# Performance work log

Hardware: AMD Instinct MI355X
Metric: run time of the kernel (lower is better)

The kernel has to match this reference:

```python
import jax, jax.numpy as jnp
import numpy as np

# ---- dims ----
N = 16380      # atoms
R = 819        # residues
APR = 20       # atoms per residue
K = 16         # k_neighbors
H = 64         # hidden_mult (channels)
HEADS = 8
DH = H // HEADS
L = 6          # hidden_layers
BINS = 100
MIN_D, MAX_D = 0.0, 10.0
E_DIM = 64     # embed_dim
FFN = 2 * H    # mlp_ratio = 2


def setup_inputs() -> dict:
    key = jax.random.key(0)
    ks = jax.random.split(key, 22)
    g = lambda k, shape, fan: jax.random.normal(k, shape, jnp.float32) / np.sqrt(fan)
    return {
        'coords': jax.random.uniform(ks[0], (N, 3), jnp.float32) * 70.0,
        'atom_ids': jax.random.randint(ks[1], (N,), 0, 64),
        'res_ids': jax.random.randint(ks[2], (N,), 0, 8),
        'elem_ids': jax.random.randint(ks[3], (N,), 0, 16),
        'residue_index': jnp.repeat(jnp.arange(R), APR),
        'emb_atom': jax.random.normal(ks[4], (64, 32), jnp.float32),
        'emb_res': jax.random.normal(ks[5], (8, 16), jnp.float32),
        'emb_elem': jax.random.normal(ks[6], (16, 16), jnp.float32),
        'Win': g(ks[7], (E_DIM, H), E_DIM),
        'Wq': g(ks[8], (L, H, H), H),
        'Wk': g(ks[9], (L, H, H), H),
        'Wv': g(ks[10], (L, H, H), H),
        'Wvec': g(ks[11], (L, H, H), H),
        'wdir': jax.random.normal(ks[12], (L, H), jnp.float32) * 0.1,
        'dist_bias': jax.random.normal(ks[13], (L, BINS, HEADS), jnp.float32) * 0.1,
        'Wo': g(ks[14], (L, H, H), H),
        'W1': g(ks[15], (L, H, FFN), H),
        'W2': g(ks[16], (L, FFN, H), FFN),
        'Wg': g(ks[17], (L, H, H), H),
        'Wout': g(ks[18], (H, 2), H),
        'bout': jnp.zeros((2,), jnp.float32),
    }


def _ln(x):
    m = jnp.mean(x, axis=-1, keepdims=True)
    v = jnp.mean((x - m) ** 2, axis=-1, keepdims=True)
    return (x - m) * jax.lax.rsqrt(v + 1e-5)


def reference(coords, atom_ids, res_ids, elem_ids, residue_index,
              emb_atom, emb_res, emb_elem, Win, Wq, Wk, Wv, Wvec, wdir,
              dist_bias, Wo, W1, W2, Wg, Wout, bout):
    n = coords.shape[0]
    # --- polymer embedding: concat atom/residue/element embeddings ---
    feat = jnp.concatenate(
        [emb_atom[atom_ids], emb_res[res_ids], emb_elem[elem_ids]], axis=-1)  # (N, E_DIM)
    # --- kNN graph via dense pairwise distances (avoid (N,N,3) intermediate) ---
    sq = jnp.sum(coords * coords, axis=-1)
    d2 = sq[:, None] + sq[None, :] - 2.0 * (coords @ coords.T)     # (N, N)
    idx = jnp.arange(n)
    d2 = d2.at[idx, idx].set(jnp.inf)
    _, nbr = jax.lax.top_k(-d2, K)                                  # (N, K) src per dst
    # --- edge geometry: relative vector, distance, bin ---
    dvec = coords[:, None, :] - coords[nbr]                         # (N, K, 3) dst - src
    d = jnp.sqrt(jnp.sum(dvec * dvec, axis=-1) + 1e-12)
    dirn = dvec / d[..., None]
    bins = jnp.clip(((d - MIN_D) / (MAX_D - MIN_D) * BINS).astype(jnp.int32), 0, BINS - 1)
    # --- lift to hidden repr: scalars from embedding, vectors start at zero ---
    s = feat @ Win                                                  # (N, H) l=0 features
    v = jnp.zeros((n, H, 3), s.dtype)                               # (N, H, 3) l=1 features
    for l in range(L):
        h = _ln(s)
        q = (h @ Wq[l]).reshape(n, HEADS, DH)
        kf = (h @ Wk[l]).reshape(n, HEADS, DH)
        vf = (h @ Wv[l]).reshape(n, HEADS, DH)
        kn, vn = kf[nbr], vf[nbr]                                   # (N, K, HEADS, DH)
        logits = jnp.einsum('nhd,nkhd->nkh', q, kn) / np.sqrt(DH) + dist_bias[l][bins]
        attn = jax.nn.softmax(logits, axis=1)                       # softmax over K nbrs
        msg = jnp.einsum('nkh,nkhd->nhd', attn, vn).reshape(n, H)
        # equivariant vector messages: mixed source vectors + edge direction term
        vvals = jnp.einsum('nhc,hg->ngc', v, Wvec[l])               # (N, H, 3)
        vmsg = vvals[nbr] + wdir[l][None, None, :, None] * dirn[:, :, None, :]
        attn_c = jnp.repeat(attn, DH, axis=-1)                      # (N, K, H)
        vagg = jnp.einsum('nkh,nkhc->nhc', attn_c, vmsg)
        s = s + msg @ Wo[l]
        v = v + vagg
        h2 = _ln(s)
        s = s + jax.nn.gelu(h2 @ W1[l]) @ W2[l]                     # scalar FFN
        v = v * jax.nn.sigmoid(h2 @ Wg[l])[..., None]               # gated vector update
    # --- out repr is l=0 only; residue mean-pool then linear head ---
    res_feat = jax.ops.segment_sum(s, residue_index, num_segments=R) / APR
    return res_feat @ Wout + bout                                   # (R, 2)
```

## Files before the change

### kernel.cpp

```cpp
#include <hip/hip_runtime.h>
#include <cfloat>

#define NN    16380
#define RR    819
#define APR   20
#define KNB   16
#define HID   64
#define LAYERS 6
#define BINS  100
#define N64   (NN*HID)

#define ATB   32
#define NBLK  512
#define LDA   68
#define LDU   132
#define CSIZE 4.375f

#define OFF_QA    0
#define OFF_KA    (1*N64)
#define OFF_FA    (2*N64)
#define OFF_QB    (3*N64)
#define OFF_KB    (4*N64)
#define OFF_FB    (5*N64)
#define OFF_VA    (6*N64)
#define OFF_VB    (9*N64)
#define OFF_S     (12*N64)
#define OFF_DIRNS (13*N64)
#define OFF_C4    (OFF_DIRNS + NN*48)
#define OFF_C4S   (OFF_C4 + NN*4)
#define OFF_RES   (OFF_C4S + NN*4)
#define OFF_NBRS  (OFF_RES + RR*64)
#define OFF_BINSS (OFF_NBRS + NN*16)
#define OFF_O2N   (OFF_BINSS + NN*16)
#define OFF_N2O   (OFF_O2N + NN)
#define OFF_CELL  (OFF_N2O + NN)
#define OFF_HIST  (OFF_CELL + NN)
#define OFF_CNT   (OFF_HIST + 4096)
#define OFF_BASE  (OFF_CNT + 4096)

typedef unsigned long long u64;
#define U64MAX 0xFFFFFFFFFFFFFFFFull

__device__ __forceinline__ float gelu_f(float x) {
    float x3 = x*x*x;
    float t = tanhf(0.7978845608028654f*(x + 0.044715f*x3));
    return 0.5f*x*(1.0f+t);
}
__device__ __forceinline__ float sigmoid_f(float x) {
    return 1.0f/(1.0f + expf(-x));
}
__device__ __forceinline__ int spread3(int x) {
    return (x&1) | ((x&2)<<2) | ((x&4)<<4) | ((x&8)<<6);
}
__device__ __forceinline__ unsigned sortable_u32(float f) {
    unsigned u = __float_as_uint(f);
    return u ^ ((u & 0x80000000u) ? 0xFFFFFFFFu : 0x80000000u);
}

__global__ void pad_cell_kernel(const float* __restrict__ coords, float4* __restrict__ c4,
                                int* __restrict__ cellid, int* __restrict__ hist,
                                float* __restrict__ resb, int n) {
    int i = blockIdx.x*256 + threadIdx.x;
    for (int j = i; j < RR*HID; j += 16384) resb[j] = 0.f;
    if (i >= n) return;
    float x = coords[3*i], y = coords[3*i+1], z = coords[3*i+2];
    float sq = __fadd_rn(__fadd_rn(__fmul_rn(x,x), __fmul_rn(y,y)), __fmul_rn(z,z));
    c4[i] = make_float4(x, y, z, sq);
    int cx = min(15, max(0, (int)(x * (16.0f/70.0f))));
    int cy = min(15, max(0, (int)(y * (16.0f/70.0f))));
    int cz = min(15, max(0, (int)(z * (16.0f/70.0f))));
    int m = spread3(cx) | (spread3(cy)<<1) | (spread3(cz)<<2);
    cellid[i] = m;
    atomicAdd(&hist[m], 1);
}
__global__ void scan_kernel(const int* __restrict__ hist, int* __restrict__ base) {
    __shared__ int part[256];
    int t = threadIdx.x;
    int loc[16]; int s = 0;
    #pragma unroll
    for (int e = 0; e < 16; ++e) { loc[e] = s; s += hist[t*16+e]; }
    part[t] = s;
    __syncthreads();
    if (t == 0) { int acc = 0; for (int i = 0; i < 256; ++i) { int v = part[i]; part[i] = acc; acc += v; } }
    __syncthreads();
    int off = part[t];
    #pragma unroll
    for (int e = 0; e < 16; ++e) base[t*16+e] = off + loc[e];
}
__global__ void scatter_kernel(const int* __restrict__ cellid, const int* __restrict__ base,
                               int* __restrict__ cnt, int* __restrict__ o2n,
                               int* __restrict__ n2o, const float4* __restrict__ c4,
                               float4* __restrict__ c4s, int n) {
    int i = blockIdx.x*256 + threadIdx.x;
    if (i >= n) return;
    int m = cellid[i];
    int pos = base[m] + atomicAdd(&cnt[m], 1);
    o2n[i] = pos; n2o[pos] = i;
    c4s[pos] = c4[i];
}

#define SCRATCH 1024
__global__ __launch_bounds__(256) void knn_grid_kernel(
    const float4* __restrict__ c4s, const int* __restrict__ base, const int* __restrict__ hist,
    const int* __restrict__ n2o, const int* __restrict__ o2n,
    int* __restrict__ nbr, int* __restrict__ binsO, float* __restrict__ dirn, int n)
{
    __shared__ int sIdx[4][SCRATCH];
    int tid = threadIdx.x;
    int wv = tid >> 6, lane = tid & 63;
    int i = blockIdx.x*4 + wv;
    bool valid = i < n;
    int ii = valid ? i : 0;
    float4 cd = c4s[ii];
    float sqd = cd.w;
    int cx = min(15, max(0, (int)(cd.x * (16.0f/70.0f))));
    int cy = min(15, max(0, (int)(cd.y * (16.0f/70.0f))));
    int cz = min(15, max(0, (int)(cd.z * (16.0f/70.0f))));
    u64 dlist = U64MAX;
    u64 vmax  = U64MAX;
    int* sidx = sIdx[wv];

    auto compute_pk = [&](int idx) -> u64 {
        if (idx == i) return U64MAX;
        float4 cc = c4s[idx];
        float dt = __fmul_rn(cd.x, cc.x);
        dt = __fmaf_rn(cd.y, cc.y, dt);
        dt = __fmaf_rn(cd.z, cc.z, dt);
        float key = __fsub_rn(__fadd_rn(sqd, cc.w), __fmul_rn(2.0f, dt));
        int org = n2o[idx];
        return ((u64)sortable_u32(key) << 32) | (unsigned)org;
    };

    auto process_batch = [&](int M) {
        if (M <= 0) return;
        u64 lmin = U64MAX;
        for (int p = lane; p < M; p += 64) {
            u64 pk = compute_pk(sidx[p]);
            lmin = (pk < lmin) ? pk : lmin;
        }
        u64 T = lmin;
        #pragma unroll
        for (int off = 1; off < 64; off <<= 1) {
            u64 o = __shfl_xor(T, off);
            T = (o > T) ? o : T;
        }
        for (int c0 = 0; c0 < M; c0 += 64) {
            int p = c0 + lane;
            u64 mypk = (p < M) ? compute_pk(sidx[p]) : U64MAX;
            u64 bound = (vmax < T) ? vmax : T;
            unsigned long long mask = __ballot(mypk <= bound);
            while (mask) {
                int lb = (int)__builtin_ctzll(mask);
                mask &= mask - 1;
                u64 dc = __shfl(mypk, lb);
                if (dc < vmax) {
                    u64 dp = __shfl_up(dlist, 1);
                    bool below = dc < dlist;
                    bool take  = below && (lane == 0 || dc >= dp);
                    if (lane < 16) dlist = below ? (take ? dc : dp) : dlist;
                    vmax = __shfl(dlist, 15);
                }
            }
        }
    };

    for (int R = 2; R <= 16; ++R) {
        int side = 2*R+1;
        int ncell = side*side*side;
        int M = 0;
        for (int t0 = 0; t0 < ncell; t0 += 64) {
            int t = t0 + lane;
            int cnt = 0, b = 0;
            if (t < ncell) {
                int dxc = t % side - R;
                int dyc = (t/side) % side - R;
                int dzc = t/(side*side) - R;
                int ch = max(abs(dxc), max(abs(dyc), abs(dzc)));
                bool use = (R == 2) || (ch == R);
                int x = cx+dxc, y = cy+dyc, z = cz+dzc;
                if (use && x>=0 && x<16 && y>=0 && y<16 && z>=0 && z<16) {
                    int m = spread3(x) | (spread3(y)<<1) | (spread3(z)<<2);
                    cnt = hist[m]; b = base[m];
                }
            }
            int incl = cnt;
            #pragma unroll
            for (int o = 1; o < 64; o <<= 1) { int v = __shfl_up(incl, o); if (lane >= o) incl += v; }
            int excl = incl - cnt;
            int tot = __shfl(incl, 63);
            if (M + tot > SCRATCH) { process_batch(M); M = 0; }
            for (int e = 0; e < cnt; ++e) {
                int pos = M + excl + e;
                if (pos < SCRATCH) sidx[pos] = b + e;
            }
            M = min(M + tot, SCRATCH);
        }
        process_batch(M);
        float rim = (float)R * CSIZE;
        unsigned thS = sortable_u32(rim*rim - 0.05f);
        if ((unsigned)(vmax >> 32) < thS) break;
    }
    if (valid && lane < 16) {
        int org = (int)(dlist & 0xFFFFFFFFull);
        int src = o2n[org];
        float4 cs = c4s[src];
        float dx = __fsub_rn(cd.x, cs.x);
        float dy = __fsub_rn(cd.y, cs.y);
        float dz = __fsub_rn(cd.z, cs.z);
        float ss = __fadd_rn(__fadd_rn(__fmul_rn(dx,dx), __fmul_rn(dy,dy)),
                             __fmul_rn(dz,dz));
        float dd = __fsqrt_rn(__fadd_rn(ss, 1e-12f));
        nbr[i*KNB + lane] = src;
        float bf = __fmul_rn(__fdiv_rn(dd, 10.0f), 100.0f);
        int b = (int)bf;
        b = min(max(b, 0), BINS-1);
        binsO[i*KNB + lane] = b;
        dirn[i*48 + lane*3 + 0] = __fdiv_rn(dx, dd);
        dirn[i*48 + lane*3 + 1] = __fdiv_rn(dy, dd);
        dirn[i*48 + lane*3 + 2] = __fdiv_rn(dz, dd);
    }
}

__global__ __launch_bounds__(256) void prologue_kernel(
    const int* __restrict__ aid, const int* __restrict__ rid, const int* __restrict__ eid,
    const int* __restrict__ n2o,
    const float* __restrict__ ea, const float* __restrict__ er, const float* __restrict__ ee,
    const float* __restrict__ Win, const float* __restrict__ Wq, const float* __restrict__ Wk,
    const float* __restrict__ Wv,
    float* __restrict__ sg, float* __restrict__ qout, float* __restrict__ kout,
    float* __restrict__ vfout)
{
    __shared__ __align__(16) float sS[ATB*LDA];
    __shared__ __align__(16) float sH[ATB*LDA];
    __shared__ __align__(16) float sW[4096];
    const int tid = threadIdx.x;
    const int a0 = blockIdx.x*ATB;
    const int gi = tid>>4, gj = tid&15;
    const int lrow = tid>>3, lsub = tid&7;

    auto stageW = [&](const float* W) {
        const float4* src = (const float4*)W; float4* dst = (float4*)sW;
        #pragma unroll
        for (int r = 0; r < 4; ++r) dst[tid + 256*r] = src[tid + 256*r];
    };
    auto do_gemm = [&](const float* sA, float4& c0, float4& c1) {
        const float* a0p = sA + gi*LDA;
        const float* a1p = sA + (gi+16)*LDA;
        const float* wr  = sW + gj*4;
        #pragma unroll 8
        for (int k = 0; k < 64; ++k) {
            float av0 = a0p[k], av1 = a1p[k];
            float4 w = *(const float4*)(wr + k*64);
            c0.x = fmaf(av0,w.x,c0.x); c0.y = fmaf(av0,w.y,c0.y);
            c0.z = fmaf(av0,w.z,c0.z); c0.w = fmaf(av0,w.w,c0.w);
            c1.x = fmaf(av1,w.x,c1.x); c1.y = fmaf(av1,w.y,c1.y);
            c1.z = fmaf(av1,w.z,c1.z); c1.w = fmaf(av1,w.w,c1.w);
        }
    };
    auto do_ln = [&](const float* src, float* dst) {
        const float* sp = src + lrow*LDA + lsub*8;
        float v[8]; float s1 = 0.f;
        #pragma unroll
        for (int e = 0; e < 8; ++e) { v[e] = sp[e]; s1 += v[e]; }
        s1 += __shfl_xor(s1,1); s1 += __shfl_xor(s1,2); s1 += __shfl_xor(s1,4);
        float mean = s1*(1.0f/64.0f);
        float s2 = 0.f;
        #pragma unroll
        for (int e = 0; e < 8; ++e) { float t = v[e]-mean; s2 += t*t; }
        s2 += __shfl_xor(s2,1); s2 += __shfl_xor(s2,2); s2 += __shfl_xor(s2,4);
        float sc = 1.0f/sqrtf(s2*(1.0f/64.0f)+1e-5f);
        float* dp = dst + lrow*LDA + lsub*8;
        #pragma unroll
        for (int e = 0; e < 8; ++e) dp[e] = (v[e]-mean)*sc;
    };
    auto store_g = [&](float* base, float4 c0, float4 c1) {
        int g0 = a0+gi, g1 = a0+gi+16;
        if (g0 < NN) *(float4*)(base + (size_t)g0*64 + gj*4) = c0;
        if (g1 < NN) *(float4*)(base + (size_t)g1*64 + gj*4) = c1;
    };

    {
        int ga = a0 + lrow;
        int io = (ga < NN) ? n2o[ga] : 0;
        #pragma unroll
        for (int e = 0; e < 8; ++e) {
            int c = lsub*8 + e;
            float x = 0.f;
            if (ga < NN) {
                if (c < 32)      x = ea[aid[io]*32 + c];
                else if (c < 48) x = er[rid[io]*16 + (c-32)];
                else             x = ee[eid[io]*16 + (c-48)];
            }
            sH[lrow*LDA + c] = x;
        }
    }
    __syncthreads();
    stageW(Win); __syncthreads();
    {
        float4 c0 = make_float4(0,0,0,0), c1 = c0;
        do_gemm(sH, c0, c1);
        *(float4*)(sS + gi*LDA + gj*4)      = c0;
        *(float4*)(sS + (gi+16)*LDA + gj*4) = c1;
        store_g(sg, c0, c1);
    }
    __syncthreads();
    do_ln(sS, sH);
    __syncthreads();
    stageW(Wk); __syncthreads();
    { float4 c0 = make_float4(0,0,0,0), c1 = c0; do_gemm(sH, c0, c1); store_g(kout, c0, c1); }
    __syncthreads();
    stageW(Wv); __syncthreads();
    { float4 c0 = make_float4(0,0,0,0), c1 = c0; do_gemm(sH, c0, c1); store_g(vfout, c0, c1); }
    __syncthreads();
    stageW(Wq); __syncthreads();
    { float4 c0 = make_float4(0,0,0,0), c1 = c0; do_gemm(sH, c0, c1); store_g(qout, c0, c1); }
}

__global__ __launch_bounds__(256) void layer_kernel(
    const float* __restrict__ qin, const float* __restrict__ kin, const float* __restrict__ vfin,
    float* __restrict__ qout, float* __restrict__ kout, float* __restrict__ vfout,
    const float* __restrict__ vin, float* __restrict__ vout,
    float* __restrict__ sg, const float* __restrict__ dirn,
    const int* __restrict__ nbr, const int* __restrict__ bins,
    float* __restrict__ resb, const int* __restrict__ ridx, const int* __restrict__ n2o,
    const float* __restrict__ Wvec, const float* __restrict__ wdir,
    const float* __restrict__ dist_bias,
    const float* __restrict__ Wo, const float* __restrict__ W1, const float* __restrict__ W2,
    const float* __restrict__ Wg, const float* __restrict__ Wq, const float* __restrict__ Wk,
    const float* __restrict__ Wv, int l)
{
    __shared__ __align__(16) float sS[ATB*LDA];
    __shared__ __align__(16) float sH[ATB*LDA];
    __shared__ __align__(16) float sM[ATB*LDU];
    __shared__ __align__(16) float sVA[3][ATB*LDA];
    __shared__ __align__(16) float sW[4096];
    __shared__ float sDS[ATB*24];

    const int tid = threadIdx.x;
    const int bswz = (blockIdx.x & 7) * (NBLK/8) + (blockIdx.x >> 3);
    const int a0 = bswz*ATB;
    const int gi = tid>>4, gj = tid&15;
    const int lrow = tid>>3, lsub = tid&7;
    const int wv = tid>>6, lane = tid&63;

    const float* Wo_l = Wo + l*4096;
    const float* Wg_l = Wg + l*4096;
    const float* Wc_l = Wvec + l*4096;
    const float* W1_l = W1 + l*8192;
    const float* W2_l = W2 + l*8192;
    const float* db_l = dist_bias + l*BINS*8;
    const float* wd_l = wdir + l*64;

    auto stageW = [&](const float* W) {
        const float4* src = (const float4*)W; float4* dst = (float4*)sW;
        #pragma unroll
        for (int r = 0; r < 4; ++r) dst[tid + 256*r] = src[tid + 256*r];
    };
    auto stageW1h = [&](const float* W1l, int h) {
        const float4* src = (const float4*)W1l; float4* dst = (float4*)sW;
        #pragma unroll
        for (int r = 0; r < 4; ++r) {
            int q = tid + 256*r;
            int row = q >> 4, c4i = q & 15;
            dst[q] = src[row*32 + h*16 + c4i];
        }
    };
    auto do_gemm = [&](const float* sA, int lda, int ko, float4& c0, float4& c1) {
        const float* a0p = sA + gi*lda + ko;
        const float* a1p = sA + (gi+16)*lda + ko;
        const float* wr  = sW + gj*4;
        #pragma unroll 8
        for (int k = 0; k < 64; ++k) {
            float av0 = a0p[k], av1 = a1p[k];
            float4 w = *(const float4*)(wr + k*64);
            c0.x = fmaf(av0,w.x,c0.x); c0.y = fmaf(av0,w.y,c0.y);
            c0.z = fmaf(av0,w.z,c0.z); c0.w = fmaf(av0,w.w,c0.w);
            c1.x = fmaf(av1,w.x,c1.x); c1.y = fmaf(av1,w.y,c1.y);
            c1.z = fmaf(av1,w.z,c1.z); c1.w = fmaf(av1,w.w,c1.w);
        }
    };
    auto do_ln = [&](const float* src, float* dst) {
        const float* sp = src + lrow*LDA + lsub*8;
        float v[8]; float s1 = 0.f;
        #pragma unroll
        for (int e = 0; e < 8; ++e) { v[e] = sp[e]; s1 += v[e]; }
        s1 += __shfl_xor(s1,1); s1 += __shfl_xor(s1,2); s1 += __shfl_xor(s1,4);
        float mean = s1*(1.0f/64.0f);
        float s2 = 0.f;
        #pragma unroll
        for (int e = 0; e < 8; ++e) { float t = v[e]-mean; s2 += t*t; }
        s2 += __shfl_xor(s2,1); s2 += __shfl_xor(s2,2); s2 += __shfl_xor(s2,4);
        float sc = 1.0f/sqrtf(s2*(1.0f/64.0f)+1e-5f);
        float* dp = dst + lrow*LDA + lsub*8;
        #pragma unroll
        for (int e = 0; e < 8; ++e) dp[e] = (v[e]-mean)*sc;
    };
    auto store_g = [&](float* base, float4 c0, float4 c1) {
        int g0 = a0+gi, g1 = a0+gi+16;
        if (g0 < NN) *(float4*)(base + (size_t)g0*64 + gj*4) = c0;
        if (g1 < NN) *(float4*)(base + (size_t)g1*64 + gj*4) = c1;
    };

    {
        int ga = a0 + lrow;
        float4 z = make_float4(0,0,0,0);
        float4 x0 = z, x1 = z;
        if (ga < NN) {
            const float4* sp = (const float4*)(sg + (size_t)ga*64);
            x0 = sp[lsub*2]; x1 = sp[lsub*2+1];
        }
        float4* dp = (float4*)(sS + lrow*LDA);
        dp[lsub*2] = x0; dp[lsub*2+1] = x1;
    }

    for (int aa = 0; aa < 8; ++aa) {
        int la = wv*8 + aa;
        int ga = a0 + la;
        if (ga >= NN) break;
        float qh = qin[(size_t)ga*64 + lane];
        float lg[KNB]; int nb[KNB];
        #pragma unroll
        for (int k = 0; k < KNB; ++k) {
            int j = nbr[ga*KNB + k];
            nb[k] = j;
            float t = qh * kin[(size_t)j*64 + lane];
            t += __shfl_xor(t,1); t += __shfl_xor(t,2); t += __shfl_xor(t,4);
            lg[k] = t*0.35355339059327373f + db_l[bins[ga*KNB+k]*8 + (lane>>3)];
        }
        float m = lg[0];
        #pragma unroll
        for (int k = 1; k < KNB; ++k) m = fmaxf(m, lg[k]);
        float ssum = 0.f;
        #pragma unroll
        for (int k = 0; k < KNB; ++k) { lg[k] = expf(lg[k]-m); ssum += lg[k]; }
        float inv = 1.0f/ssum;
        float mh=0.f, b0=0.f, b1=0.f, b2=0.f, s0=0.f, s1=0.f, s2=0.f;
        if (l > 0) {
            #pragma unroll
            for (int k = 0; k < KNB; ++k) {
                float w = lg[k]*inv; int j = nb[k];
                mh += w * vfin[(size_t)j*64 + lane];
                b0 += w * vin[(size_t)j*64 + lane];
                b1 += w * vin[(size_t)N64 + (size_t)j*64 + lane];
                b2 += w * vin[2*(size_t)N64 + (size_t)j*64 + lane];
                s0 += w * dirn[ga*48 + k*3 + 0];
                s1 += w * dirn[ga*48 + k*3 + 1];
                s2 += w * dirn[ga*48 + k*3 + 2];
            }
            sVA[0][la*LDA + lane] = b0;
            sVA[1][la*LDA + lane] = b1;
            sVA[2][la*LDA + lane] = b2;
        } else {
            #pragma unroll
            for (int k = 0; k < KNB; ++k) {
                float w = lg[k]*inv; int j = nb[k];
                mh += w * vfin[(size_t)j*64 + lane];
                s0 += w * dirn[ga*48 + k*3 + 0];
                s1 += w * dirn[ga*48 + k*3 + 1];
                s2 += w * dirn[ga*48 + k*3 + 2];
            }
        }
        sM[la*LDU + lane] = mh;
        if ((lane & 7) == 0) {
            int hh = lane >> 3;
            sDS[la*24 + 0*8 + hh] = s0;
            sDS[la*24 + 1*8 + hh] = s1;
            sDS[la*24 + 2*8 + hh] = s2;
        }
    }
    __syncthreads();

    stageW(Wo_l); __syncthreads();
    {
        float4 c0 = *(float4*)(sS + gi*LDA + gj*4);
        float4 c1 = *(float4*)(sS + (gi+16)*LDA + gj*4);
        do_gemm(sM, LDU, 0, c0, c1);
        __syncthreads();
        *(float4*)(sS + gi*LDA + gj*4)      = c0;
        *(float4*)(sS + (gi+16)*LDA + gj*4) = c1;
    }
    __syncthreads();

    do_ln(sS, sH);
    __syncthreads();

    stageW(Wg_l); __syncthreads();
    {
        float4 g0 = make_float4(0,0,0,0), g1 = g0;
        do_gemm(sH, LDA, 0, g0, g1);
        g0.x=sigmoid_f(g0.x); g0.y=sigmoid_f(g0.y); g0.z=sigmoid_f(g0.z); g0.w=sigmoid_f(g0.w);
        g1.x=sigmoid_f(g1.x); g1.y=sigmoid_f(g1.y); g1.z=sigmoid_f(g1.z); g1.w=sigmoid_f(g1.w);
        __syncthreads();
        stageW(Wc_l); __syncthreads();
        float4 wd4 = *(const float4*)&wd_l[gj*4];
        int g0i = a0+gi, g1i = a0+gi+16;
        #pragma unroll
        for (int p = 0; p < 3; ++p) {
            float4 t0 = make_float4(0,0,0,0), t1 = t0;
            if (l > 0) do_gemm(sVA[p], LDA, 0, t0, t1);
            float sp0 = sDS[gi*24 + p*8 + (gj>>1)];
            float sp1 = sDS[(gi+16)*24 + p*8 + (gj>>1)];
            if (g0i < NN) {
                float4 vi = make_float4(0,0,0,0);
                if (l > 0) vi = *(const float4*)(vin + (size_t)p*N64 + (size_t)g0i*64 + gj*4);
                float4 o;
                o.x = (vi.x + t0.x + wd4.x*sp0)*g0.x;
                o.y = (vi.y + t0.y + wd4.y*sp0)*g0.y;
                o.z = (vi.z + t0.z + wd4.z*sp0)*g0.z;
                o.w = (vi.w + t0.w + wd4.w*sp0)*g0.w;
                *(float4*)(vout + (size_t)p*N64 + (size_t)g0i*64 + gj*4) = o;
            }
            if (g1i < NN) {
                float4 vi = make_float4(0,0,0,0);
                if (l > 0) vi = *(const float4*)(vin + (size_t)p*N64 + (size_t)g1i*64 + gj*4);
                float4 o;
                o.x = (vi.x + t1.x + wd4.x*sp1)*g1.x;
                o.y = (vi.y + t1.y + wd4.y*sp1)*g1.y;
                o.z = (vi.z + t1.z + wd4.z*sp1)*g1.z;
                o.w = (vi.w + t1.w + wd4.w*sp1)*g1.w;
                *(float4*)(vout + (size_t)p*N64 + (size_t)g1i*64 + gj*4) = o;
            }
        }
    }
    __syncthreads();

    stageW1h(W1_l, 0); __syncthreads();
    {
        float4 c0 = make_float4(0,0,0,0), c1 = c0;
        do_gemm(sH, LDA, 0, c0, c1);
        c0.x=gelu_f(c0.x); c0.y=gelu_f(c0.y); c0.z=gelu_f(c0.z); c0.w=gelu_f(c0.w);
        c1.x=gelu_f(c1.x); c1.y=gelu_f(c1.y); c1.z=gelu_f(c1.z); c1.w=gelu_f(c1.w);
        __syncthreads();
        *(float4*)(sM + gi*LDU + gj*4)      = c0;
        *(float4*)(sM + (gi+16)*LDU + gj*4) = c1;
    }
    __syncthreads();
    stageW1h(W1_l, 1); __syncthreads();
    {
        float4 c0 = make_float4(0,0,0,0), c1 = c0;
        do_gemm(sH, LDA, 0, c0, c1);
        c0.x=gelu_f(c0.x); c0.y=gelu_f(c0.y); c0.z=gelu_f(c0.z); c0.w=gelu_f(c0.w);
        c1.x=gelu_f(c1.x); c1.y=gelu_f(c1.y); c1.z=gelu_f(c1.z); c1.w=gelu_f(c1.w);
        __syncthreads();
        *(float4*)(sM + gi*LDU + 64 + gj*4)      = c0;
        *(float4*)(sM + (gi+16)*LDU + 64 + gj*4) = c1;
    }
    __syncthreads();
    stageW(W2_l); __syncthreads();
    {
        float4 c0 = *(float4*)(sS + gi*LDA + gj*4);
        float4 c1 = *(float4*)(sS + (gi+16)*LDA + gj*4);
        do_gemm(sM, LDU, 0, c0, c1);
        __syncthreads();
        stageW(W2_l + 4096); __syncthreads();
        do_gemm(sM, LDU, 64, c0, c1);
        __syncthreads();
        *(float4*)(sS + gi*LDA + gj*4)      = c0;
        *(float4*)(sS + (gi+16)*LDA + gj*4) = c1;
    }
    __syncthreads();

    if (l < LAYERS-1) {
        do_ln(sS, sH);
        __syncthreads();
        stageW(Wk + (l+1)*4096); __syncthreads();
        { float4 c0 = make_float4(0,0,0,0), c1 = c0; do_gemm(sH, LDA, 0, c0, c1); store_g(kout, c0, c1); }
        __syncthreads();
        stageW(Wv + (l+1)*4096); __syncthreads();
        { float4 c0 = make_float4(0,0,0,0), c1 = c0; do_gemm(sH, LDA, 0, c0, c1); store_g(vfout, c0, c1); }
        __syncthreads();
        stageW(Wq + (l+1)*4096); __syncthreads();
        { float4 c0 = make_float4(0,0,0,0), c1 = c0; do_gemm(sH, LDA, 0, c0, c1); store_g(qout, c0, c1); }
        {
            int ga = a0 + lrow;
            if (ga < NN) {
                float4* dp = (float4*)(sg + (size_t)ga*64);
                const float4* sp = (const float4*)(sS + lrow*LDA);
                dp[lsub*2] = sp[lsub*2]; dp[lsub*2+1] = sp[lsub*2+1];
            }
        }
    } else {
        int ga = a0 + lrow;
        if (ga < NN) {
            int r = ridx[n2o[ga]];
            #pragma unroll
            for (int e = 0; e < 8; ++e)
                atomicAdd(&resb[r*64 + lsub*8 + e], sS[lrow*LDA + lsub*8 + e]);
        }
    }
}

__global__ void head_kernel(const float* __restrict__ res, const float* __restrict__ Wout,
                            const float* __restrict__ bout, float* __restrict__ out, int r_total) {
    int wave = threadIdx.x >> 6, lane = threadIdx.x & 63;
    int r = blockIdx.x*4 + wave;
    if (r >= r_total) return;
    float p = res[r*HID + lane] * (1.0f/APR);
    float o0 = p * Wout[lane*2 + 0];
    float o1 = p * Wout[lane*2 + 1];
    #pragma unroll
    for (int off = 1; off < 64; off <<= 1) { o0 += __shfl_xor(o0, off); o1 += __shfl_xor(o1, off); }
    if (lane == 0) { out[r*2+0] = o0 + bout[0]; out[r*2+1] = o1 + bout[1]; }
}

extern "C" void kernel_launch(void* const* d_in, const int* in_sizes, int n_in,
                              void* d_out, int out_size, void* d_ws, size_t ws_size,
                              hipStream_t stream) {
    const float* coords    = (const float*)d_in[0];
    const int*   atom_ids  = (const int*)d_in[1];
    const int*   res_ids   = (const int*)d_in[2];
    const int*   elem_ids  = (const int*)d_in[3];
    const int*   ridx      = (const int*)d_in[4];
    const float* emb_atom  = (const float*)d_in[5];
    const float* emb_res   = (const float*)d_in[6];
    const float* emb_elem  = (const float*)d_in[7];
    const float* Win       = (const float*)d_in[8];
    const float* Wq        = (const float*)d_in[9];
    const float* Wk        = (const float*)d_in[10];
    const float* Wv        = (const float*)d_in[11];
    const float* Wvec      = (const float*)d_in[12];
    const float* wdir      = (const float*)d_in[13];
    const float* dist_bias = (const float*)d_in[14];
    const float* Wo        = (const float*)d_in[15];
    const float* W1        = (const float*)d_in[16];
    const float* W2        = (const float*)d_in[17];
    const float* Wg        = (const float*)d_in[18];
    const float* Wout      = (const float*)d_in[19];
    const float* bout      = (const float*)d_in[20];
    float* out = (float*)d_out;

    float* ws = (float*)d_ws;
    float* qA = ws + OFF_QA;  float* kA = ws + OFF_KA;  float* fA = ws + OFF_FA;
    float* qB = ws + OFF_QB;  float* kB = ws + OFF_KB;  float* fB = ws + OFF_FB;
    float* vA = ws + OFF_VA;  float* vB = ws + OFF_VB;
    float* sg = ws + OFF_S;
    float* dirn_s = ws + OFF_DIRNS;
    float4* c4  = (float4*)(ws + OFF_C4);
    float4* c4s = (float4*)(ws + OFF_C4S);
    float* resb = ws + OFF_RES;
    int* nbr_s  = (int*)(ws + OFF_NBRS);
    int* bins_s = (int*)(ws + OFF_BINSS);
    int* o2n    = (int*)(ws + OFF_O2N);
    int* n2o    = (int*)(ws + OFF_N2O);
    int* cellid = (int*)(ws + OFF_CELL);
    int* hist   = (int*)(ws + OFF_HIST);
    int* cnt    = (int*)(ws + OFF_CNT);
    int* baseb  = (int*)(ws + OFF_BASE);

    hipMemsetAsync(hist, 0, 2*4096*sizeof(int), stream);

    pad_cell_kernel<<<(NN+255)/256, 256, 0, stream>>>(coords, c4, cellid, hist, resb, NN);
    scan_kernel<<<1, 256, 0, stream>>>(hist, baseb);
    scatter_kernel<<<(NN+255)/256, 256, 0, stream>>>(cellid, baseb, cnt, o2n, n2o, c4, c4s, NN);
    knn_grid_kernel<<<(NN+3)/4, 256, 0, stream>>>(c4s, baseb, hist, n2o, o2n, nbr_s, bins_s, dirn_s, NN);

    prologue_kernel<<<NBLK, 256, 0, stream>>>(atom_ids, res_ids, elem_ids, n2o,
                                              emb_atom, emb_res, emb_elem,
                                              Win, Wq, Wk, Wv, sg, qA, kA, fA);
    for (int l = 0; l < LAYERS; ++l) {
        int p = l & 1;
        const float* qin = p ? qB : qA;  float* qout = p ? qA : qB;
        const float* kin = p ? kB : kA;  float* kout = p ? kA : kB;
        const float* fin = p ? fB : fA;  float* fout = p ? fA : fB;
        const float* vin = p ? vB : vA;  float* vout = p ? vA : vB;
        layer_kernel<<<NBLK, 256, 0, stream>>>(qin, kin, fin, qout, kout, fout,
                                               vin, vout, sg, dirn_s, nbr_s, bins_s,
                                               resb, ridx, n2o,
                                               Wvec, wdir, dist_bias,
                                               Wo, W1, W2, Wg, Wq, Wk, Wv, l);
    }
    head_kernel<<<(RR+3)/4, 256, 0, stream>>>(resb, Wout, bout, out, RR);
}
```

Before: 620.6 us.

## Fuse prologue, all layers and head into one persistent kernel with grid barriers

Merges the prologue, the six per-layer launches and the head kernel into a single persistent kernel of 512 blocks. Between stages it uses an atomic counter and generation software grid barrier in workspace, which is zeroed by the extended memset. This removes seven kernel launch gaps and tail drains. In exchange it depends on all 512 blocks being co-resident to avoid deadlock, and it spins on global atomics at every layer boundary.

```diff
diff --git a/kernel.cpp b/kernel.cpp
--- a/kernel.cpp
+++ b/kernel.cpp
@@ -37,6 +37,7 @@
 #define OFF_HIST  (OFF_CELL + NN)
 #define OFF_CNT   (OFF_HIST + 4096)
 #define OFF_BASE  (OFF_CNT + 4096)
+#define OFF_BAR   (OFF_BASE + 4096)
 
 typedef unsigned long long u64;
 #define U64MAX 0xFFFFFFFFFFFFFFFFull
@@ -221,31 +222,53 @@
     }
 }
 
-__global__ __launch_bounds__(256) void prologue_kernel(
+__global__ __launch_bounds__(256) void mega_kernel(
     const int* __restrict__ aid, const int* __restrict__ rid, const int* __restrict__ eid,
-    const int* __restrict__ n2o,
+    const int* __restrict__ n2o, const int* __restrict__ ridx,
     const float* __restrict__ ea, const float* __restrict__ er, const float* __restrict__ ee,
     const float* __restrict__ Win, const float* __restrict__ Wq, const float* __restrict__ Wk,
-    const float* __restrict__ Wv,
-    float* __restrict__ sg, float* __restrict__ qout, float* __restrict__ kout,
-    float* __restrict__ vfout)
+    const float* __restrict__ Wv, const float* __restrict__ Wvec, const float* __restrict__ wdir,
+    const float* __restrict__ dist_bias, const float* __restrict__ Wo,
+    const float* __restrict__ W1, const float* __restrict__ W2, const float* __restrict__ Wg,
+    const float* __restrict__ Wout, const float* __restrict__ bout,
+    float* __restrict__ qA, float* __restrict__ kA, float* __restrict__ fA,
+    float* __restrict__ qB, float* __restrict__ kB, float* __restrict__ fB,
+    float* __restrict__ vA, float* __restrict__ vB,
+    float* __restrict__ sg, const float* __restrict__ dirn,
+    const int* __restrict__ nbr, const int* __restrict__ bins,
+    float* __restrict__ resb, unsigned* __restrict__ bar, float* __restrict__ out)
 {
     __shared__ __align__(16) float sS[ATB*LDA];
     __shared__ __align__(16) float sH[ATB*LDA];
+    __shared__ __align__(16) float sM[ATB*LDU];
+    __shared__ __align__(16) float sVA[3][ATB*LDA];
     __shared__ __align__(16) float sW[4096];
+    __shared__ float sDS[ATB*24];
+
     const int tid = threadIdx.x;
-    const int a0 = blockIdx.x*ATB;
+    const int bswz = (blockIdx.x & 7) * (NBLK/8) + (blockIdx.x >> 3);
+    const int a0 = bswz*ATB;
     const int gi = tid>>4, gj = tid&15;
     const int lrow = tid>>3, lsub = tid&7;
+    const int wv = tid>>6, lane = tid&63;
 
     auto stageW = [&](const float* W) {
         const float4* src = (const float4*)W; float4* dst = (float4*)sW;
         #pragma unroll
         for (int r = 0; r < 4; ++r) dst[tid + 256*r] = src[tid + 256*r];
     };
-    auto do_gemm = [&](const float* sA, float4& c0, float4& c1) {
-        const float* a0p = sA + gi*LDA;
-        const float* a1p = sA + (gi+16)*LDA;
+    auto stageW1h = [&](const float* W1l, int h) {
+        const float4* src = (const float4*)W1l; float4* dst = (float4*)sW;
+        #pragma unroll
+        for (int r = 0; r < 4; ++r) {
+            int q = tid + 256*r;
+            int row = q >> 4, c4i = q & 15;
+            dst[q] = src[row*32 + h*16 + c4i];
+        }
+    };
+    auto do_gemm = [&](const float* sA, int lda, int ko, float4& c0, float4& c1) {
+        const float* a0p = sA + gi*lda + ko;
+        const float* a1p = sA + (gi+16)*lda + ko;
         const float* wr  = sW + gj*4;
         #pragma unroll 8
         for (int k = 0; k < 64; ++k) {
@@ -278,6 +301,23 @@
         if (g0 < NN) *(float4*)(base + (size_t)g0*64 + gj*4) = c0;
         if (g1 < NN) *(float4*)(base + (size_t)g1*64 + gj*4) = c1;
     };
+    auto grid_sync = [&]() {
+        __syncthreads();
+        __threadfence();
+        if (tid == 0) {
+            unsigned* cnt = bar; unsigned* gen = bar+1;
+            unsigned g = __hip_atomic_load(gen, __ATOMIC_RELAXED, __HIP_MEMORY_SCOPE_AGENT);
+            unsigned arr = __hip_atomic_fetch_add(cnt, 1u, __ATOMIC_ACQ_REL, __HIP_MEMORY_SCOPE_AGENT);
+            if (arr == (unsigned)(NBLK-1)) {
+                __hip_atomic_store(cnt, 0u, __ATOMIC_RELAXED, __HIP_MEMORY_SCOPE_AGENT);
+                __hip_atomic_fetch_add(gen, 1u, __ATOMIC_RELEASE, __HIP_MEMORY_SCOPE_AGENT);
+            } else {
+                while (__hip_atomic_load(gen, __ATOMIC_ACQUIRE, __HIP_MEMORY_SCOPE_AGENT) == g) {}
+            }
+        }
+        __syncthreads();
+        __threadfence();
+    };
 
     {
         int ga = a0 + lrow;
@@ -298,7 +338,7 @@
     stageW(Win); __syncthreads();
     {
         float4 c0 = make_float4(0,0,0,0), c1 = c0;
-        do_gemm(sH, c0, c1);
+        do_gemm(sH, LDA, 0, c0, c1);
         *(float4*)(sS + gi*LDA + gj*4)      = c0;
         *(float4*)(sS + (gi+16)*LDA + gj*4) = c1;
         store_g(sg, c0, c1);
@@ -307,300 +347,237 @@
     do_ln(sS, sH);
     __syncthreads();
     stageW(Wk); __syncthreads();
-    { float4 c0 = make_float4(0,0,0,0), c1 = c0; do_gemm(sH, c0, c1); store_g(kout, c0, c1); }
+    { float4 c0 = make_float4(0,0,0,0), c1 = c0; do_gemm(sH, LDA, 0, c0, c1); store_g(kA, c0, c1); }
     __syncthreads();
     stageW(Wv); __syncthreads();
-    { float4 c0 = make_float4(0,0,0,0), c1 = c0; do_gemm(sH, c0, c1); store_g(vfout, c0, c1); }
+    { float4 c0 = make_float4(0,0,0,0), c1 = c0; do_gemm(sH, LDA, 0, c0, c1); store_g(fA, c0, c1); }
     __syncthreads();
     stageW(Wq); __syncthreads();
-    { float4 c0 = make_float4(0,0,0,0), c1 = c0; do_gemm(sH, c0, c1); store_g(qout, c0, c1); }
-}
-
-__global__ __launch_bounds__(256) void layer_kernel(
-    const float* __restrict__ qin, const float* __restrict__ kin, const float* __restrict__ vfin,
-    float* __restrict__ qout, float* __restrict__ kout, float* __restrict__ vfout,
-    const float* __restrict__ vin, float* __restrict__ vout,
-    float* __restrict__ sg, const float* __restrict__ dirn,
-    const int* __restrict__ nbr, const int* __restrict__ bins,
-    float* __restrict__ resb, const int* __restrict__ ridx, const int* __restrict__ n2o,
-    const float* __restrict__ Wvec, const float* __restrict__ wdir,
-    const float* __restrict__ dist_bias,
-    const float* __restrict__ Wo, const float* __restrict__ W1, const float* __restrict__ W2,
-    const float* __restrict__ Wg, const float* __restrict__ Wq, const float* __restrict__ Wk,
-    const float* __restrict__ Wv, int l)
-{
-    __shared__ __align__(16) float sS[ATB*LDA];
-    __shared__ __align__(16) float sH[ATB*LDA];
-    __shared__ __align__(16) float sM[ATB*LDU];
-    __shared__ __align__(16) float sVA[3][ATB*LDA];
-    __shared__ __align__(16) float sW[4096];
-    __shared__ float sDS[ATB*24];
-
-    const int tid = threadIdx.x;
-    const int bswz = (blockIdx.x & 7) * (NBLK/8) + (blockIdx.x >> 3);
-    const int a0 = bswz*ATB;
-    const int gi = tid>>4, gj = tid&15;
-    const int lrow = tid>>3, lsub = tid&7;
-    const int wv = tid>>6, lane = tid&63;
-
-    const float* Wo_l = Wo + l*4096;
-    const float* Wg_l = Wg + l*4096;
-    const float* Wc_l = Wvec + l*4096;
-    const float* W1_l = W1 + l*8192;
-    const float* W2_l = W2 + l*8192;
-    const float* db_l = dist_bias + l*BINS*8;
-    const float* wd_l = wdir + l*64;
-
-    auto stageW = [&](const float* W) {
-        const float4* src = (const float4*)W; float4* dst = (float4*)sW;
-        #pragma unroll
-        for (int r = 0; r < 4; ++r) dst[tid + 256*r] = src[tid + 256*r];
-    };
-    auto stageW1h = [&](const float* W1l, int h) {
-        const float4* src = (const float4*)W1l; float4* dst = (float4*)sW;
-        #pragma unroll
-        for (int r = 0; r < 4; ++r) {
-            int q = tid + 256*r;
-            int row = q >> 4, c4i = q & 15;
-            dst[q] = src[row*32 + h*16 + c4i];
-        }
-    };
-    auto do_gemm = [&](const float* sA, int lda, int ko, float4& c0, float4& c1) {
-        const float* a0p = sA + gi*lda + ko;
-        const float* a1p = sA + (gi+16)*lda + ko;
-        const float* wr  = sW + gj*4;
-        #pragma unroll 8
-        for (int k = 0; k < 64; ++k) {
-            float av0 = a0p[k], av1 = a1p[k];
-            float4 w = *(const float4*)(wr + k*64);
-            c0.x = fmaf(av0,w.x,c0.x); c0.y = fmaf(av0,w.y,c0.y);
-            c0.z = fmaf(av0,w.z,c0.z); c0.w = fmaf(av0,w.w,c0.w);
-            c1.x = fmaf(av1,w.x,c1.x); c1.y = fmaf(av1,w.y,c1.y);
-            c1.z = fmaf(av1,w.z,c1.z); c1.w = fmaf(av1,w.w,c1.w);
-        }
-    };
-    auto do_ln = [&](const float* src, float* dst) {
-        const float* sp = src + lrow*LDA + lsub*8;
-        float v[8]; float s1 = 0.f;
-        #pragma unroll
-        for (int e = 0; e < 8; ++e) { v[e] = sp[e]; s1 += v[e]; }
-        s1 += __shfl_xor(s1,1); s1 += __shfl_xor(s1,2); s1 += __shfl_xor(s1,4);
-        float mean = s1*(1.0f/64.0f);
-        float s2 = 0.f;
-        #pragma unroll
-        for (int e = 0; e < 8; ++e) { float t = v[e]-mean; s2 += t*t; }
-        s2 += __shfl_xor(s2,1); s2 += __shfl_xor(s2,2); s2 += __shfl_xor(s2,4);
-        float sc = 1.0f/sqrtf(s2*(1.0f/64.0f)+1e-5f);
-        float* dp = dst + lrow*LDA + lsub*8;
-        #pragma unroll
-        for (int e = 0; e < 8; ++e) dp[e] = (v[e]-mean)*sc;
-    };
-    auto store_g = [&](float* base, float4 c0, float4 c1) {
-        int g0 = a0+gi, g1 = a0+gi+16;
-        if (g0 < NN) *(float4*)(base + (size_t)g0*64 + gj*4) = c0;
-        if (g1 < NN) *(float4*)(base + (size_t)g1*64 + gj*4) = c1;
-    };
-
-    {
-        int ga = a0 + lrow;
-        float4 z = make_float4(0,0,0,0);
-        float4 x0 = z, x1 = z;
-        if (ga < NN) {
-            const float4* sp = (const float4*)(sg + (size_t)ga*64);
-            x0 = sp[lsub*2]; x1 = sp[lsub*2+1];
-        }
-        float4* dp = (float4*)(sS + lrow*LDA);
-        dp[lsub*2] = x0; dp[lsub*2+1] = x1;
-    }
-
-    for (int aa = 0; aa < 8; ++aa) {
-        int la = wv*8 + aa;
-        int ga = a0 + la;
-        if (ga >= NN) break;
-        float qh = qin[(size_t)ga*64 + lane];
-        float lg[KNB]; int nb[KNB];
-        #pragma unroll
-        for (int k = 0; k < KNB; ++k) {
-            int j = nbr[ga*KNB + k];
-            nb[k] = j;
-            float t = qh * kin[(size_t)j*64 + lane];
-            t += __shfl_xor(t,1); t += __shfl_xor(t,2); t += __shfl_xor(t,4);
-            lg[k] = t*0.35355339059327373f + db_l[bins[ga*KNB+k]*8 + (lane>>3)];
-        }
-        float m = lg[0];
-        #pragma unroll
-        for (int k = 1; k < KNB; ++k) m = fmaxf(m, lg[k]);
-        float ssum = 0.f;
-        #pragma unroll
-        for (int k = 0; k < KNB; ++k) { lg[k] = expf(lg[k]-m); ssum += lg[k]; }
-        float inv = 1.0f/ssum;
-        float mh=0.f, b0=0.f, b1=0.f, b2=0.f, s0=0.f, s1=0.f, s2=0.f;
-        if (l > 0) {
+    { float4 c0 = make_float4(0,0,0,0), c1 = c0; do_gemm(sH, LDA, 0, c0, c1); store_g(qA, c0, c1); }
+
+    grid_sync();
+
+    for (int l = 0; l < LAYERS; ++l) {
+        int par = l & 1;
+        const float* qin  = par ? qB : qA;
+        const float* kin  = par ? kB : kA;
+        const float* vfin = par ? fB : fA;
+        float* qout = par ? qA : qB;
+        float* kout = par ? kA : kB;
+        float* vfout= par ? fA : fB;
+        const float* vin = par ? vB : vA;
+        float* vout      = par ? vA : vB;
+
+        const float* Wo_l = Wo + l*4096;
+        const float* Wg_l = Wg + l*4096;
+        const float* Wc_l = Wvec + l*4096;
+        const float* W1_l = W1 + l*8192;
+        const float* W2_l = W2 + l*8192;
+        const float* db_l = dist_bias + l*BINS*8;
+        const float* wd_l = wdir + l*64;
+
+        {
+            int ga = a0 + lrow;
+            float4 z = make_float4(0,0,0,0);
+            float4 x0 = z, x1 = z;
+            if (ga < NN) {
+                const float4* sp = (const float4*)(sg + (size_t)ga*64);
+                x0 = sp[lsub*2]; x1 = sp[lsub*2+1];
+            }
+            float4* dp = (float4*)(sS + lrow*LDA);
+            dp[lsub*2] = x0; dp[lsub*2+1] = x1;
+        }
+
+        for (int aa = 0; aa < 8; ++aa) {
+            int la = wv*8 + aa;
+            int ga = a0 + la;
+            if (ga >= NN) break;
+            float qh = qin[(size_t)ga*64 + lane];
+            float lg[KNB]; int nb[KNB];
             #pragma unroll
             for (int k = 0; k < KNB; ++k) {
-                float w = lg[k]*inv; int j = nb[k];
-                mh += w * vfin[(size_t)j*64 + lane];
-                b0 += w * vin[(size_t)j*64 + lane];
-                b1 += w * vin[(size_t)N64 + (size_t)j*64 + lane];
-                b2 += w * vin[2*(size_t)N64 + (size_t)j*64 + lane];
-                s0 += w * dirn[ga*48 + k*3 + 0];
-                s1 += w * dirn[ga*48 + k*3 + 1];
-                s2 += w * dirn[ga*48 + k*3 + 2];
-            }
-            sVA[0][la*LDA + lane] = b0;
-            sVA[1][la*LDA + lane] = b1;
-            sVA[2][la*LDA + lane] = b2;
+                int j = nbr[ga*KNB + k];
+                nb[k] = j;
+                float t = qh * kin[(size_t)j*64 + lane];
+                t += __shfl_xor(t,1); t += __shfl_xor(t,2); t += __shfl_xor(t,4);
+                lg[k] = t*0.35355339059327373f + db_l[bins[ga*KNB+k]*8 + (lane>>3)];
+            }
+            float m = lg[0];
+            #pragma unroll
+            for (int k = 1; k < KNB; ++k) m = fmaxf(m, lg[k]);
+            float ssum = 0.f;
+            #pragma unroll
+            for (int k = 0; k < KNB; ++k) { lg[k] = expf(lg[k]-m); ssum += lg[k]; }
+            float inv = 1.0f/ssum;
+            float mh=0.f, b0=0.f, b1=0.f, b2=0.f, s0=0.f, s1=0.f, s2=0.f;
+            if (l > 0) {
+                #pragma unroll
+                for (int k = 0; k < KNB; ++k) {
+                    float w = lg[k]*inv; int j = nb[k];
+                    mh += w * vfin[(size_t)j*64 + lane];
+                    b0 += w * vin[(size_t)j*64 + lane];
+                    b1 += w * vin[(size_t)N64 + (size_t)j*64 + lane];
+                    b2 += w * vin[2*(size_t)N64 + (size_t)j*64 + lane];
+                    s0 += w * dirn[ga*48 + k*3 + 0];
+                    s1 += w * dirn[ga*48 + k*3 + 1];
+                    s2 += w * dirn[ga*48 + k*3 + 2];
+                }
+                sVA[0][la*LDA + lane] = b0;
+                sVA[1][la*LDA + lane] = b1;
+                sVA[2][la*LDA + lane] = b2;
+            } else {
+                #pragma unroll
+                for (int k = 0; k < KNB; ++k) {
+                    float w = lg[k]*inv; int j = nb[k];
+                    mh += w * vfin[(size_t)j*64 + lane];
+                    s0 += w * dirn[ga*48 + k*3 + 0];
+                    s1 += w * dirn[ga*48 + k*3 + 1];
+                    s2 += w * dirn[ga*48 + k*3 + 2];
+                }
+            }
+            sM[la*LDU + lane] = mh;
+            if ((lane & 7) == 0) {
+                int hh = lane >> 3;
+                sDS[la*24 + 0*8 + hh] = s0;
+                sDS[la*24 + 1*8 + hh] = s1;
+                sDS[la*24 + 2*8 + hh] = s2;
+            }
+        }
+        __syncthreads();
+
+        stageW(Wo_l); __syncthreads();
+        {
+            float4 c0 = *(float4*)(sS + gi*LDA + gj*4);
+            float4 c1 = *(float4*)(sS + (gi+16)*LDA + gj*4);
+            do_gemm(sM, LDU, 0, c0, c1);
+            __syncthreads();
+            *(float4*)(sS + gi*LDA + gj*4)      = c0;
+            *(float4*)(sS + (gi+16)*LDA + gj*4) = c1;
+        }
+        __syncthreads();
+
+        do_ln(sS, sH);
+        __syncthreads();
+
+        stageW(Wg_l); __syncthreads();
+        {
+            float4 g0 = make_float4(0,0,0,0), g1 = g0;
+            do_gemm(sH, LDA, 0, g0, g1);
+            g0.x=sigmoid_f(g0.x); g0.y=sigmoid_f(g0.y); g0.z=sigmoid_f(g0.z); g0.w=sigmoid_f(g0.w);
+            g1.x=sigmoid_f(g1.x); g1.y=sigmoid_f(g1.y); g1.z=sigmoid_f(g1.z); g1.w=sigmoid_f(g1.w);
+            __syncthreads();
+            stageW(Wc_l); __syncthreads();
+            float4 wd4 = *(const float4*)&wd_l[gj*4];
+            int g0i = a0+gi, g1i = a0+gi+16;
+            #pragma unroll
+            for (int p = 0; p < 3; ++p) {
+                float4 t0 = make_float4(0,0,0,0), t1 = t0;
+                if (l > 0) do_gemm(sVA[p], LDA, 0, t0, t1);
+                float sp0 = sDS[gi*24 + p*8 + (gj>>1)];
+                float sp1 = sDS[(gi+16)*24 + p*8 + (gj>>1)];
+                if (g0i < NN) {
+                    float4 vi = make_float4(0,0,0,0);
+                    if (l > 0) vi = *(const float4*)(vin + (size_t)p*N64 + (size_t)g0i*64 + gj*4);
+                    float4 o;
+                    o.x = (vi.x + t0.x + wd4.x*sp0)*g0.x;
+                    o.y = (vi.y + t0.y + wd4.y*sp0)*g0.y;
+                    o.z = (vi.z + t0.z + wd4.z*sp0)*g0.z;
+                    o.w = (vi.w + t0.w + wd4.w*sp0)*g0.w;
+                    *(float4*)(vout + (size_t)p*N64 + (size_t)g0i*64 + gj*4) = o;
+                }
+                if (g1i < NN) {
+                    float4 vi = make_float4(0,0,0,0);
+                    if (l > 0) vi = *(const float4*)(vin + (size_t)p*N64 + (size_t)g1i*64 + gj*4);
+                    float4 o;
+                    o.x = (vi.x + t1.x + wd4.x*sp1)*g1.x;
+                    o.y = (vi.y + t1.y + wd4.y*sp1)*g1.y;
+                    o.z = (vi.z + t1.z + wd4.z*sp1)*g1.z;
+                    o.w = (vi.w + t1.w + wd4.w*sp1)*g1.w;
+                    *(float4*)(vout + (size_t)p*N64 + (size_t)g1i*64 + gj*4) = o;
+                }
+            }
+        }
+        __syncthreads();
+
+        stageW1h(W1_l, 0); __syncthreads();
+        {
+            float4 c0 = make_float4(0,0,0,0), c1 = c0;
+            do_gemm(sH, LDA, 0, c0, c1);
+            c0.x=gelu_f(c0.x); c0.y=gelu_f(c0.y); c0.z=gelu_f(c0.z); c0.w=gelu_f(c0.w);
+            c1.x=gelu_f(c1.x); c1.y=gelu_f(c1.y); c1.z=gelu_f(c1.z); c1.w=gelu_f(c1.w);
+            __syncthreads();
+            *(float4*)(sM + gi*LDU + gj*4)      = c0;
+            *(float4*)(sM + (gi+16)*LDU + gj*4) = c1;
+        }
+        __syncthreads();
+        stageW1h(W1_l, 1); __syncthreads();
+        {
+            float4 c0 = make_float4(0,0,0,0), c1 = c0;
+            do_gemm(sH, LDA, 0, c0, c1);
+            c0.x=gelu_f(c0.x); c0.y=gelu_f(c0.y); c0.z=gelu_f(c0.z); c0.w=gelu_f(c0.w);
+            c1.x=gelu_f(c1.x); c1.y=gelu_f(c1.y); c1.z=gelu_f(c1.z); c1.w=gelu_f(c1.w);
+            __syncthreads();
+            *(float4*)(sM + gi*LDU + 64 + gj*4)      = c0;
+            *(float4*)(sM + (gi+16)*LDU + 64 + gj*4) = c1;
+        }
+        __syncthreads();
+        stageW(W2_l); __syncthreads();
+        {
+            float4 c0 = *(float4*)(sS + gi*LDA + gj*4);
+            float4 c1 = *(float4*)(sS + (gi+16)*LDA + gj*4);
+            do_gemm(sM, LDU, 0, c0, c1);
+            __syncthreads();
+            stageW(W2_l + 4096); __syncthreads();
+            do_gemm(sM, LDU, 64, c0, c1);
+            __syncthreads();
+            *(float4*)(sS + gi*LDA + gj*4)      = c0;
+            *(float4*)(sS + (gi+16)*LDA + gj*4) = c1;
+        }
+        __syncthreads();
+
+        if (l < LAYERS-1) {
+            do_ln(sS, sH);
+            __syncthreads();
+            stageW(Wk + (l+1)*4096); __syncthreads();
+            { float4 c0 = make_float4(0,0,0,0), c1 = c0; do_gemm(sH, LDA, 0, c0, c1); store_g(kout, c0, c1); }
+            __syncthreads();
+            stageW(Wv + (l+1)*4096); __syncthreads();
+            { float4 c0 = make_float4(0,0,0,0), c1 = c0; do_gemm(sH, LDA, 0, c0, c1); store_g(vfout, c0, c1); }
+            __syncthreads();
+            stageW(Wq + (l+1)*4096); __syncthreads();
+            { float4 c0 = make_float4(0,0,0,0), c1 = c0; do_gemm(sH, LDA, 0, c0, c1); store_g(qout, c0, c1); }
+            {
+                int ga = a0 + lrow;
+                if (ga < NN) {
+                    float4* dp = (float4*)(sg + (size_t)ga*64);
+                    const float4* sp = (const float4*)(sS + lrow*LDA);
+                    dp[lsub*2] = sp[lsub*2]; dp[lsub*2+1] = sp[lsub*2+1];
+                }
+            }
         } else {
-            #pragma unroll
-            for (int k = 0; k < KNB; ++k) {
-                float w = lg[k]*inv; int j = nb[k];
-                mh += w * vfin[(size_t)j*64 + lane];
-                s0 += w * dirn[ga*48 + k*3 + 0];
-                s1 += w * dirn[ga*48 + k*3 + 1];
-                s2 += w * dirn[ga*48 + k*3 + 2];
-            }
-        }
-        sM[la*LDU + lane] = mh;
-        if ((lane & 7) == 0) {
-            int hh = lane >> 3;
-            sDS[la*24 + 0*8 + hh] = s0;
-            sDS[la*24 + 1*8 + hh] = s1;
-            sDS[la*24 + 2*8 + hh] = s2;
-        }
-    }
-    __syncthreads();
-
-    stageW(Wo_l); __syncthreads();
-    {
-        float4 c0 = *(float4*)(sS + gi*LDA + gj*4);
-        float4 c1 = *(float4*)(sS + (gi+16)*LDA + gj*4);
-        do_gemm(sM, LDU, 0, c0, c1);
-        __syncthreads();
-        *(float4*)(sS + gi*LDA + gj*4)      = c0;
-        *(float4*)(sS + (gi+16)*LDA + gj*4) = c1;
-    }
-    __syncthreads();
-
-    do_ln(sS, sH);
-    __syncthreads();
-
-    stageW(Wg_l); __syncthreads();
-    {
-        float4 g0 = make_float4(0,0,0,0), g1 = g0;
-        do_gemm(sH, LDA, 0, g0, g1);
-        g0.x=sigmoid_f(g0.x); g0.y=sigmoid_f(g0.y); g0.z=sigmoid_f(g0.z); g0.w=sigmoid_f(g0.w);
-        g1.x=sigmoid_f(g1.x); g1.y=sigmoid_f(g1.y); g1.z=sigmoid_f(g1.z); g1.w=sigmoid_f(g1.w);
-        __syncthreads();
-        stageW(Wc_l); __syncthreads();
-        float4 wd4 = *(const float4*)&wd_l[gj*4];
-        int g0i = a0+gi, g1i = a0+gi+16;
-        #pragma unroll
-        for (int p = 0; p < 3; ++p) {
-            float4 t0 = make_float4(0,0,0,0), t1 = t0;
-            if (l > 0) do_gemm(sVA[p], LDA, 0, t0, t1);
-            float sp0 = sDS[gi*24 + p*8 + (gj>>1)];
-            float sp1 = sDS[(gi+16)*24 + p*8 + (gj>>1)];
-            if (g0i < NN) {
-                float4 vi = make_float4(0,0,0,0);
-                if (l > 0) vi = *(const float4*)(vin + (size_t)p*N64 + (size_t)g0i*64 + gj*4);
-                float4 o;
-                o.x = (vi.x + t0.x + wd4.x*sp0)*g0.x;
-                o.y = (vi.y + t0.y + wd4.y*sp0)*g0.y;
-                o.z = (vi.z + t0.z + wd4.z*sp0)*g0.z;
-                o.w = (vi.w + t0.w + wd4.w*sp0)*g0.w;
-                *(float4*)(vout + (size_t)p*N64 + (size_t)g0i*64 + gj*4) = o;
-            }
-            if (g1i < NN) {
-                float4 vi = make_float4(0,0,0,0);
-                if (l > 0) vi = *(const float4*)(vin + (size_t)p*N64 + (size_t)g1i*64 + gj*4);
-                float4 o;
-                o.x = (vi.x + t1.x + wd4.x*sp1)*g1.x;
-                o.y = (vi.y + t1.y + wd4.y*sp1)*g1.y;
-                o.z = (vi.z + t1.z + wd4.z*sp1)*g1.z;
-                o.w = (vi.w + t1.w + wd4.w*sp1)*g1.w;
-                *(float4*)(vout + (size_t)p*N64 + (size_t)g1i*64 + gj*4) = o;
-            }
-        }
-    }
-    __syncthreads();
-
-    stageW1h(W1_l, 0); __syncthreads();
-    {
-        float4 c0 = make_float4(0,0,0,0), c1 = c0;
-        do_gemm(sH, LDA, 0, c0, c1);
-        c0.x=gelu_f(c0.x); c0.y=gelu_f(c0.y); c0.z=gelu_f(c0.z); c0.w=gelu_f(c0.w);
-        c1.x=gelu_f(c1.x); c1.y=gelu_f(c1.y); c1.z=gelu_f(c1.z); c1.w=gelu_f(c1.w);
-        __syncthreads();
-        *(float4*)(sM + gi*LDU + gj*4)      = c0;
-        *(float4*)(sM + (gi+16)*LDU + gj*4) = c1;
-    }
-    __syncthreads();
-    stageW1h(W1_l, 1); __syncthreads();
-    {
-        float4 c0 = make_float4(0,0,0,0), c1 = c0;
-        do_gemm(sH, LDA, 0, c0, c1);
-        c0.x=gelu_f(c0.x); c0.y=gelu_f(c0.y); c0.z=gelu_f(c0.z); c0.w=gelu_f(c0.w);
-        c1.x=gelu_f(c1.x); c1.y=gelu_f(c1.y); c1.z=gelu_f(c1.z); c1.w=gelu_f(c1.w);
-        __syncthreads();
-        *(float4*)(sM + gi*LDU + 64 + gj*4)      = c0;
-        *(float4*)(sM + (gi+16)*LDU + 64 + gj*4) = c1;
-    }
-    __syncthreads();
-    stageW(W2_l); __syncthreads();
-    {
-        float4 c0 = *(float4*)(sS + gi*LDA + gj*4);
-        float4 c1 = *(float4*)(sS + (gi+16)*LDA + gj*4);
-        do_gemm(sM, LDU, 0, c0, c1);
-        __syncthreads();
-        stageW(W2_l + 4096); __syncthreads();
-        do_gemm(sM, LDU, 64, c0, c1);
-        __syncthreads();
-        *(float4*)(sS + gi*LDA + gj*4)      = c0;
-        *(float4*)(sS + (gi+16)*LDA + gj*4) = c1;
-    }
-    __syncthreads();
-
-    if (l < LAYERS-1) {
-        do_ln(sS, sH);
-        __syncthreads();
-        stageW(Wk + (l+1)*4096); __syncthreads();
-        { float4 c0 = make_float4(0,0,0,0), c1 = c0; do_gemm(sH, LDA, 0, c0, c1); store_g(kout, c0, c1); }
-        __syncthreads();
-        stageW(Wv + (l+1)*4096); __syncthreads();
-        { float4 c0 = make_float4(0,0,0,0), c1 = c0; do_gemm(sH, LDA, 0, c0, c1); store_g(vfout, c0, c1); }
-        __syncthreads();
-        stageW(Wq + (l+1)*4096); __syncthreads();
-        { float4 c0 = make_float4(0,0,0,0), c1 = c0; do_gemm(sH, LDA, 0, c0, c1); store_g(qout, c0, c1); }
-        {
             int ga = a0 + lrow;
             if (ga < NN) {
-                float4* dp = (float4*)(sg + (size_t)ga*64);
-                const float4* sp = (const float4*)(sS + lrow*LDA);
-                dp[lsub*2] = sp[lsub*2]; dp[lsub*2+1] = sp[lsub*2+1];
-            }
-        }
-    } else {
-        int ga = a0 + lrow;
-        if (ga < NN) {
-            int r = ridx[n2o[ga]];
+                int r = ridx[n2o[ga]];
+                #pragma unroll
+                for (int e = 0; e < 8; ++e)
+                    atomicAdd(&resb[r*64 + lsub*8 + e], sS[lrow*LDA + lsub*8 + e]);
+            }
+        }
+
+        grid_sync();
+    }
+
+    {
+        int r = blockIdx.x*4 + wv;
+        if (blockIdx.x < (RR+3)/4 && r < RR) {
+            float p = resb[r*HID + lane] * (1.0f/APR);
+            float o0 = p * Wout[lane*2 + 0];
+            float o1 = p * Wout[lane*2 + 1];
             #pragma unroll
-            for (int e = 0; e < 8; ++e)
-                atomicAdd(&resb[r*64 + lsub*8 + e], sS[lrow*LDA + lsub*8 + e]);
+            for (int off = 1; off < 64; off <<= 1) { o0 += __shfl_xor(o0, off); o1 += __shfl_xor(o1, off); }
+            if (lane == 0) { out[r*2+0] = o0 + bout[0]; out[r*2+1] = o1 + bout[1]; }
         }
     }
-}
-
-__global__ void head_kernel(const float* __restrict__ res, const float* __restrict__ Wout,
-                            const float* __restrict__ bout, float* __restrict__ out, int r_total) {
-    int wave = threadIdx.x >> 6, lane = threadIdx.x & 63;
-    int r = blockIdx.x*4 + wave;
-    if (r >= r_total) return;
-    float p = res[r*HID + lane] * (1.0f/APR);
-    float o0 = p * Wout[lane*2 + 0];
-    float o1 = p * Wout[lane*2 + 1];
-    #pragma unroll
-    for (int off = 1; off < 64; off <<= 1) { o0 += __shfl_xor(o0, off); o1 += __shfl_xor(o1, off); }
-    if (lane == 0) { out[r*2+0] = o0 + bout[0]; out[r*2+1] = o1 + bout[1]; }
 }
 
 extern "C" void kernel_launch(void* const* d_in, const int* in_sizes, int n_in,
@@ -646,28 +623,19 @@
     int* hist   = (int*)(ws + OFF_HIST);
     int* cnt    = (int*)(ws + OFF_CNT);
     int* baseb  = (int*)(ws + OFF_BASE);
-
-    hipMemsetAsync(hist, 0, 2*4096*sizeof(int), stream);
+    unsigned* bar = (unsigned*)(ws + OFF_BAR);
+
+    hipMemsetAsync(hist, 0, (3*4096 + 2)*sizeof(int), stream);
 
     pad_cell_kernel<<<(NN+255)/256, 256, 0, stream>>>(coords, c4, cellid, hist, resb, NN);
     scan_kernel<<<1, 256, 0, stream>>>(hist, baseb);
     scatter_kernel<<<(NN+255)/256, 256, 0, stream>>>(cellid, baseb, cnt, o2n, n2o, c4, c4s, NN);
     knn_grid_kernel<<<(NN+3)/4, 256, 0, stream>>>(c4s, baseb, hist, n2o, o2n, nbr_s, bins_s, dirn_s, NN);
 
-    prologue_kernel<<<NBLK, 256, 0, stream>>>(atom_ids, res_ids, elem_ids, n2o,
-                                              emb_atom, emb_res, emb_elem,
-                                              Win, Wq, Wk, Wv, sg, qA, kA, fA);
-    for (int l = 0; l < LAYERS; ++l) {
-        int p = l & 1;
-        const float* qin = p ? qB : qA;  float* qout = p ? qA : qB;
-        const float* kin = p ? kB : kA;  float* kout = p ? kA : kB;
-        const float* fin = p ? fB : fA;  float* fout = p ? fA : fB;
-        const float* vin = p ? vB : vA;  float* vout = p ? vA : vB;
-        layer_kernel<<<NBLK, 256, 0, stream>>>(qin, kin, fin, qout, kout, fout,
-                                               vin, vout, sg, dirn_s, nbr_s, bins_s,
-                                               resb, ridx, n2o,
-                                               Wvec, wdir, dist_bias,
-                                               Wo, W1, W2, Wg, Wq, Wk, Wv, l);
-    }
-    head_kernel<<<(RR+3)/4, 256, 0, stream>>>(resb, Wout, bout, out, RR);
-}
+    mega_kernel<<<NBLK, 256, 0, stream>>>(atom_ids, res_ids, elem_ids, n2o, ridx,
+                                          emb_atom, emb_res, emb_elem,
+                                          Win, Wq, Wk, Wv, Wvec, wdir, dist_bias,
+                                          Wo, W1, W2, Wg, Wout, bout,
+                                          qA, kA, fA, qB, kB, fB, vA, vB,
+                                          sg, dirn_s, nbr_s, bins_s, resb, bar, out);
+}
```

Result: slower. 1.941 ms (+212.8%).
